# Kernel tuning notes

Hardware: AMD Instinct MI355X
Metric: run time of the kernel (lower is better)

The kernel has to match this reference:

```python
import jax, jax.numpy as jnp
import numpy as np

IN_FEATURES = 256
OUT_FEATURES = 512
NUM_SEGMENTS = 8
GRID_MIN, GRID_MAX = -1.0, 1.0
STEP = (GRID_MAX - GRID_MIN) / NUM_SEGMENTS
LN_EPS = 1e-5


def setup_inputs() -> dict:
    key = jax.random.key(0)
    k1, k2 = jax.random.split(key)
    B = 2048
    x = jax.random.normal(k1, (B, IN_FEATURES), dtype=jnp.float32)
    # Xavier-uniform a_embed, zeros b_embed, as in reset_parameters
    vocab = IN_FEATURES * NUM_SEGMENTS
    limit = float(np.sqrt(6.0 / (vocab + OUT_FEATURES)))
    a_weight = jax.random.uniform(k2, (vocab, OUT_FEATURES), minval=-limit, maxval=limit, dtype=jnp.float32)
    b_weight = jnp.zeros((vocab, OUT_FEATURES), dtype=jnp.float32)
    gamma = jnp.ones((IN_FEATURES,), dtype=jnp.float32)
    beta = jnp.zeros((IN_FEATURES,), dtype=jnp.float32)
    return {"x": x, "a_weight": a_weight, "b_weight": b_weight, "gamma": gamma, "beta": beta}


def reference(x, a_weight, b_weight, gamma, beta):
    # LayerNorm over in_features
    mu = jnp.mean(x, axis=-1, keepdims=True)
    var = jnp.mean(jnp.square(x - mu), axis=-1, keepdims=True)
    xn = (x - mu) * jax.lax.rsqrt(var + LN_EPS) * gamma + beta  # [B, I]

    # data-dependent segment index (torch .long() truncates; clamp makes trunc==floor here)
    float_idx = (xn - GRID_MIN) / STEP
    seg = jnp.clip(float_idx.astype(jnp.int32), 0, NUM_SEGMENTS - 1)  # [B, I]
    global_idx = seg + jnp.arange(IN_FEATURES, dtype=jnp.int32)[None, :] * NUM_SEGMENTS

    a_vals = a_weight[global_idx]  # [B, I, O]
    b_vals = b_weight[global_idx]  # [B, I, O]
    # sum over in_features of a*x + b
    y = jnp.einsum('bi,bio->bo', xn, a_vals) + jnp.sum(b_vals, axis=1)
    return y
```

## Files before the change

### kernel.cpp

```cpp
#include <hip/hip_runtime.h>

#define I_FEAT 256
#define O_FEAT 512
#define NSEG   8
#define KDIM   (I_FEAT * NSEG)
#define KTOT   (2 * KDIM)
#define KC_N   (KTOT / 32)

typedef _Float16 half8   __attribute__((ext_vector_type(8)));
typedef float    floatx4 __attribute__((ext_vector_type(4)));
typedef uint32_t uintx4  __attribute__((ext_vector_type(4)));

__global__ __launch_bounds__(256) void ln_meta(
    const float* __restrict__ x,
    const float* __restrict__ gamma,
    const float* __restrict__ beta,
    uint32_t* __restrict__ meta_g,
    int Bn)
{
    __shared__ float s_psum[4];
    __shared__ float s_psq[4];

    const int tid  = threadIdx.x;
    const int row0 = blockIdx.x * 2;
    const int wave = tid >> 6;
    const int lr   = tid >> 7;
    const int lt   = tid & 127;
    const int row  = row0 + lr;

    float v0 = 0.f, v1 = 0.f;
    if (row < Bn) {
        const float* xr = x + (size_t)row * I_FEAT;
        v0 = xr[lt];
        v1 = xr[lt + 128];
    }
    float sum = v0 + v1;
    float sq  = v0 * v0 + v1 * v1;
    #pragma unroll
    for (int d = 32; d > 0; d >>= 1) {
        sum += __shfl_down(sum, d);
        sq  += __shfl_down(sq, d);
    }
    if ((tid & 63) == 0) { s_psum[wave] = sum; s_psq[wave] = sq; }
    __syncthreads();
    if (row >= Bn) return;

    const float fsum = s_psum[2 * lr] + s_psum[2 * lr + 1];
    const float fsq  = s_psq[2 * lr]  + s_psq[2 * lr + 1];
    const float mu   = fsum * (1.0f / I_FEAT);
    const float var  = fsq * (1.0f / I_FEAT) - mu * mu;
    const float rs   = rsqrtf(var + 1e-5f);

    uint32_t* mr = meta_g + (size_t)row * I_FEAT;
    #pragma unroll
    for (int h = 0; h < 2; ++h) {
        const int f = lt + h * 128;
        const float v = h ? v1 : v0;
        float xn = (v - mu) * rs * gamma[f] + beta[f];
        float fi = (xn + 1.0f) * 4.0f;
        int seg = (int)fi;
        seg = seg < 0 ? 0 : (seg > NSEG - 1 ? NSEG - 1 : seg);
        _Float16 hx = (_Float16)xn;
        uint32_t hb = (uint32_t)__builtin_bit_cast(unsigned short, hx);
        mr[f] = ((uint32_t)seg << 16) | hb;
    }
}

__global__ __launch_bounds__(256) void pack_bfrag(
    const float* __restrict__ Aw,
    const float* __restrict__ Bw,
    uint4* __restrict__ Bf)
{
    __shared__ unsigned short T[64][72];
    const int t  = threadIdx.x;
    const int n0 = blockIdx.x * 64;
    const int k0 = blockIdx.y * 64;
    const float* src = (k0 < KDIM) ? (Aw + (size_t)k0 * O_FEAT)
                                   : (Bw + (size_t)(k0 - KDIM) * O_FEAT);

    #pragma unroll
    for (int s = 0; s < 4; ++s) {
        int e  = s * 1024 + t * 4;
        int kl = e >> 6, nl = e & 63;
        const float4 v = *(const float4*)(src + (size_t)kl * O_FEAT + n0 + nl);
        T[nl + 0][kl] = __builtin_bit_cast(unsigned short, (_Float16)v.x);
        T[nl + 1][kl] = __builtin_bit_cast(unsigned short, (_Float16)v.y);
        T[nl + 2][kl] = __builtin_bit_cast(unsigned short, (_Float16)v.z);
        T[nl + 3][kl] = __builtin_bit_cast(unsigned short, (_Float16)v.w);
    }
    __syncthreads();

    const int lane = t & 63, lane16 = lane & 15, quad = lane >> 4;
    const int sub  = t >> 6;
    #pragma unroll
    for (int f = 0; f < 2; ++f) {
        const int combo = sub * 2 + f;
        const int n16g  = combo & 3;
        const int kch   = combo >> 2;
        const int nl = n16g * 16 + lane16;
        const int kl = kch * 32 + quad * 8;
        const uint4 val = *(const uint4*)&T[nl][kl];
        const int n16t = (n0 >> 4) + n16g;
        const int kc   = (k0 >> 5) + kch;
        Bf[((size_t)n16t * KC_N + kc) * 64 + lane] = val;
    }
}

__global__ __launch_bounds__(256) void am_pack(
    const uint32_t* __restrict__ meta_g,
    uint2* __restrict__ Am,
    int Bn, int mt16Tot)
{
    const int gid  = blockIdx.x * 256 + threadIdx.x;
    const int lane = gid & 63;
    const int pc   = gid >> 6;
    const int kcp  = pc & 63;
    const int mt16 = pc >> 6;
    if (mt16 >= mt16Tot) return;
    const int m    = mt16 * 16 + (lane & 15);
    const int quad = lane >> 4;

    uint2 v = make_uint2(0u, 0u);
    if (m < Bn) {
        const uint32_t* mr = meta_g + (size_t)m * I_FEAT;
        #pragma unroll
        for (int h = 0; h < 2; ++h) {
            const int w    = (kcp * 2 + h) * 4 + quad;
            const int part = w >> 8;
            const int i    = w & 255;
            const uint32_t u = mr[i];
            const uint32_t val = part ? ((u & 0xFFFF0000u) | 0x3C00u) : u;
            if (h == 0) v.x = val; else v.y = val;
        }
    }
    Am[gid] = v;
}

static __device__ __forceinline__ half8 build_onehot(uint32_t u) {
    const uint32_t xb  = u & 0xFFFFu;
    const uint32_t seg = u >> 16;
    const uint64_t oh  = (uint64_t)xb << ((seg & 3u) << 4);
    const uint64_t lo  = (seg < 4u) ? oh : 0ull;
    const uint64_t hi  = (seg < 4u) ? 0ull : oh;
    uintx4 w;
    w[0] = (uint32_t)lo; w[1] = (uint32_t)(lo >> 32);
    w[2] = (uint32_t)hi; w[3] = (uint32_t)(hi >> 32);
    return __builtin_bit_cast(half8, w);
}

__global__ __launch_bounds__(256, 4) void kan_gemm(
    const uint2* __restrict__ Am,
    const uint4* __restrict__ Bf,
    float* __restrict__ out,
    int Bn)
{
    __shared__ float s_red[3][16][64];

    const int t      = threadIdx.x;
    const int wave   = t >> 6, lane = t & 63;
    const int lane16 = lane & 15, quad = lane >> 4;
    const int bid    = blockIdx.x;
    const int ot     = bid & 15;
    const int rt     = bid >> 4;

    const uint2* pa0 = Am + ((size_t)(rt * 2 + 0) * 64) * 64 + lane;
    const uint2* pa1 = Am + ((size_t)(rt * 2 + 1) * 64) * 64 + lane;
    const uint4* pb0 = Bf + ((size_t)(ot * 2 + 0) * KC_N) * 64 + lane;
    const uint4* pb1 = Bf + ((size_t)(ot * 2 + 1) * KC_N) * 64 + lane;

    floatx4 acc[2][2] = {};
    const int kcp0 = wave * 16;

    #pragma unroll 4
    for (int p = 0; p < 16; ++p) {
        const int kcp = kcp0 + p;
        const uint2 u0   = pa0[(size_t)kcp * 64];
        const uint2 u1   = pa1[(size_t)kcp * 64];
        const uint4 bv00 = pb0[(size_t)(2 * kcp + 0) * 64];
        const uint4 bv01 = pb0[(size_t)(2 * kcp + 1) * 64];
        const uint4 bv10 = pb1[(size_t)(2 * kcp + 0) * 64];
        const uint4 bv11 = pb1[(size_t)(2 * kcp + 1) * 64];
        {
            const half8 a0 = build_onehot(u0.x);
            const half8 a1 = build_onehot(u1.x);
            const half8 b0 = __builtin_bit_cast(half8, bv00);
            const half8 b1 = __builtin_bit_cast(half8, bv10);
            acc[0][0] = __builtin_amdgcn_mfma_f32_16x16x32_f16(a0, b0, acc[0][0], 0, 0, 0);
            acc[0][1] = __builtin_amdgcn_mfma_f32_16x16x32_f16(a0, b1, acc[0][1], 0, 0, 0);
            acc[1][0] = __builtin_amdgcn_mfma_f32_16x16x32_f16(a1, b0, acc[1][0], 0, 0, 0);
            acc[1][1] = __builtin_amdgcn_mfma_f32_16x16x32_f16(a1, b1, acc[1][1], 0, 0, 0);
        }
        {
            const half8 a0 = build_onehot(u0.y);
            const half8 a1 = build_onehot(u1.y);
            const half8 b0 = __builtin_bit_cast(half8, bv01);
            const half8 b1 = __builtin_bit_cast(half8, bv11);
            acc[0][0] = __builtin_amdgcn_mfma_f32_16x16x32_f16(a0, b0, acc[0][0], 0, 0, 0);
            acc[0][1] = __builtin_amdgcn_mfma_f32_16x16x32_f16(a0, b1, acc[0][1], 0, 0, 0);
            acc[1][0] = __builtin_amdgcn_mfma_f32_16x16x32_f16(a1, b0, acc[1][0], 0, 0, 0);
            acc[1][1] = __builtin_amdgcn_mfma_f32_16x16x32_f16(a1, b1, acc[1][1], 0, 0, 0);
        }
    }

    if (wave != 0) {
        #pragma unroll
        for (int sm = 0; sm < 2; ++sm)
            #pragma unroll
            for (int sn = 0; sn < 2; ++sn)
                #pragma unroll
                for (int r = 0; r < 4; ++r)
                    s_red[wave - 1][(sm * 2 + sn) * 4 + r][lane] = acc[sm][sn][r];
    }
    __syncthreads();
    if (wave == 0) {
        #pragma unroll
        for (int sm = 0; sm < 2; ++sm) {
            #pragma unroll
            for (int sn = 0; sn < 2; ++sn) {
                #pragma unroll
                for (int r = 0; r < 4; ++r) {
                    const int idx = (sm * 2 + sn) * 4 + r;
                    const float v = acc[sm][sn][r]
                                  + s_red[0][idx][lane]
                                  + s_red[1][idx][lane]
                                  + s_red[2][idx][lane];
                    const int grow = rt * 32 + sm * 16 + quad * 4 + r;
                    const int gcol = ot * 32 + sn * 16 + lane16;
                    if (grow < Bn)
                        out[(size_t)grow * O_FEAT + gcol] = v;
                }
            }
        }
    }
}

extern "C" void kernel_launch(void* const* d_in, const int* in_sizes, int n_in,
                              void* d_out, int out_size, void* d_ws, size_t ws_size,
                              hipStream_t stream) {
    const float* x   = (const float*)d_in[0];
    const float* Aw  = (const float*)d_in[1];
    const float* Bw  = (const float*)d_in[2];
    const float* gam = (const float*)d_in[3];
    const float* bet = (const float*)d_in[4];
    float* out       = (float*)d_out;

    const int Bn       = in_sizes[0] / I_FEAT;
    const int rt32Tot  = (Bn + 31) / 32;
    const int mt16Tot  = rt32Tot * 2;

    uint4* Bf        = (uint4*)d_ws;
    uint2* Am        = (uint2*)(Bf + (size_t)(O_FEAT / 16) * KC_N * 64);
    uint32_t* meta_g = (uint32_t*)(Am + (size_t)mt16Tot * 64 * 64);

    hipLaunchKernelGGL(ln_meta, dim3((Bn + 1) / 2), dim3(256), 0, stream,
                       x, gam, bet, meta_g, Bn);
    hipLaunchKernelGGL(pack_bfrag, dim3(O_FEAT / 64, KTOT / 64), dim3(256), 0, stream,
                       Aw, Bw, Bf);
    hipLaunchKernelGGL(am_pack, dim3(mt16Tot * 16), dim3(256), 0, stream,
                       meta_g, Am, Bn, mt16Tot);
    hipLaunchKernelGGL(kan_gemm, dim3(16 * rt32Tot), dim3(256), 0, stream,
                       Am, Bf, out, Bn);
}
```

Baseline: 91.38 us.

## Fuse prep kernels into one launch and enlarge GEMM row tile to 64

Merges the LayerNorm/meta, weight-fragment packing and A-fragment packing kernels into a single launch. Different block ranges do weight packing or row normalisation plus A packing through shared memory, which removes the meta_g round trip and two launches. The GEMM now computes 64 rows per block instead of 32, reusing each B fragment across four A tiles. It also adds a block-index swizzle for L2 locality, a reduction in which all waves share the epilogue, and launch bounds lowered to 2. The larger tile raises register pressure and cuts the number of blocks, which may hurt occupancy.

```diff
diff --git a/kernel.cpp b/kernel.cpp
--- a/kernel.cpp
+++ b/kernel.cpp
@@ -11,129 +11,118 @@
 typedef float    floatx4 __attribute__((ext_vector_type(4)));
 typedef uint32_t uintx4  __attribute__((ext_vector_type(4)));
 
-__global__ __launch_bounds__(256) void ln_meta(
+__global__ __launch_bounds__(256) void prep(
     const float* __restrict__ x,
+    const float* __restrict__ Aw,
+    const float* __restrict__ Bw,
     const float* __restrict__ gamma,
     const float* __restrict__ beta,
-    uint32_t* __restrict__ meta_g,
-    int Bn)
+    uint4* __restrict__ Bf,
+    uint2* __restrict__ Am,
+    int Bn, int pbTot)
 {
-    __shared__ float s_psum[4];
-    __shared__ float s_psq[4];
-
-    const int tid  = threadIdx.x;
-    const int row0 = blockIdx.x * 2;
-    const int wave = tid >> 6;
-    const int lr   = tid >> 7;
-    const int lt   = tid & 127;
-    const int row  = row0 + lr;
-
-    float v0 = 0.f, v1 = 0.f;
-    if (row < Bn) {
-        const float* xr = x + (size_t)row * I_FEAT;
-        v0 = xr[lt];
-        v1 = xr[lt + 128];
-    }
-    float sum = v0 + v1;
-    float sq  = v0 * v0 + v1 * v1;
-    #pragma unroll
-    for (int d = 32; d > 0; d >>= 1) {
-        sum += __shfl_down(sum, d);
-        sq  += __shfl_down(sq, d);
-    }
-    if ((tid & 63) == 0) { s_psum[wave] = sum; s_psq[wave] = sq; }
-    __syncthreads();
-    if (row >= Bn) return;
-
-    const float fsum = s_psum[2 * lr] + s_psum[2 * lr + 1];
-    const float fsq  = s_psq[2 * lr]  + s_psq[2 * lr + 1];
-    const float mu   = fsum * (1.0f / I_FEAT);
-    const float var  = fsq * (1.0f / I_FEAT) - mu * mu;
-    const float rs   = rsqrtf(var + 1e-5f);
-
-    uint32_t* mr = meta_g + (size_t)row * I_FEAT;
-    #pragma unroll
-    for (int h = 0; h < 2; ++h) {
-        const int f = lt + h * 128;
-        const float v = h ? v1 : v0;
-        float xn = (v - mu) * rs * gamma[f] + beta[f];
-        float fi = (xn + 1.0f) * 4.0f;
-        int seg = (int)fi;
-        seg = seg < 0 ? 0 : (seg > NSEG - 1 ? NSEG - 1 : seg);
-        _Float16 hx = (_Float16)xn;
-        uint32_t hb = (uint32_t)__builtin_bit_cast(unsigned short, hx);
-        mr[f] = ((uint32_t)seg << 16) | hb;
-    }
-}
-
-__global__ __launch_bounds__(256) void pack_bfrag(
-    const float* __restrict__ Aw,
-    const float* __restrict__ Bw,
-    uint4* __restrict__ Bf)
-{
-    __shared__ unsigned short T[64][72];
-    const int t  = threadIdx.x;
-    const int n0 = blockIdx.x * 64;
-    const int k0 = blockIdx.y * 64;
-    const float* src = (k0 < KDIM) ? (Aw + (size_t)k0 * O_FEAT)
-                                   : (Bw + (size_t)(k0 - KDIM) * O_FEAT);
-
-    #pragma unroll
-    for (int s = 0; s < 4; ++s) {
-        int e  = s * 1024 + t * 4;
-        int kl = e >> 6, nl = e & 63;
-        const float4 v = *(const float4*)(src + (size_t)kl * O_FEAT + n0 + nl);
-        T[nl + 0][kl] = __builtin_bit_cast(unsigned short, (_Float16)v.x);
-        T[nl + 1][kl] = __builtin_bit_cast(unsigned short, (_Float16)v.y);
-        T[nl + 2][kl] = __builtin_bit_cast(unsigned short, (_Float16)v.z);
-        T[nl + 3][kl] = __builtin_bit_cast(unsigned short, (_Float16)v.w);
-    }
-    __syncthreads();
-
-    const int lane = t & 63, lane16 = lane & 15, quad = lane >> 4;
-    const int sub  = t >> 6;
-    #pragma unroll
-    for (int f = 0; f < 2; ++f) {
-        const int combo = sub * 2 + f;
-        const int n16g  = combo & 3;
-        const int kch   = combo >> 2;
-        const int nl = n16g * 16 + lane16;
-        const int kl = kch * 32 + quad * 8;
-        const uint4 val = *(const uint4*)&T[nl][kl];
-        const int n16t = (n0 >> 4) + n16g;
-        const int kc   = (k0 >> 5) + kch;
-        Bf[((size_t)n16t * KC_N + kc) * 64 + lane] = val;
-    }
-}
-
-__global__ __launch_bounds__(256) void am_pack(
-    const uint32_t* __restrict__ meta_g,
-    uint2* __restrict__ Am,
-    int Bn, int mt16Tot)
-{
-    const int gid  = blockIdx.x * 256 + threadIdx.x;
-    const int lane = gid & 63;
-    const int pc   = gid >> 6;
-    const int kcp  = pc & 63;
-    const int mt16 = pc >> 6;
-    if (mt16 >= mt16Tot) return;
-    const int m    = mt16 * 16 + (lane & 15);
-    const int quad = lane >> 4;
-
-    uint2 v = make_uint2(0u, 0u);
-    if (m < Bn) {
-        const uint32_t* mr = meta_g + (size_t)m * I_FEAT;
-        #pragma unroll
-        for (int h = 0; h < 2; ++h) {
-            const int w    = (kcp * 2 + h) * 4 + quad;
-            const int part = w >> 8;
-            const int i    = w & 255;
-            const uint32_t u = mr[i];
-            const uint32_t val = part ? ((u & 0xFFFF0000u) | 0x3C00u) : u;
-            if (h == 0) v.x = val; else v.y = val;
-        }
-    }
-    Am[gid] = v;
+    __shared__ char smem[16 * 260 * 4];
+    const int t   = threadIdx.x;
+    const int bid = blockIdx.x;
+
+    if (bid < pbTot) {
+        unsigned short (*T)[72] = (unsigned short(*)[72])smem;
+        const int n0 = (bid & 7) * 64;
+        const int k0 = (bid >> 3) * 64;
+        const float* src = (k0 < KDIM) ? (Aw + (size_t)k0 * O_FEAT)
+                                       : (Bw + (size_t)(k0 - KDIM) * O_FEAT);
+        #pragma unroll
+        for (int s = 0; s < 4; ++s) {
+            int e  = s * 1024 + t * 4;
+            int kl = e >> 6, nl = e & 63;
+            const float4 v = *(const float4*)(src + (size_t)kl * O_FEAT + n0 + nl);
+            T[nl + 0][kl] = __builtin_bit_cast(unsigned short, (_Float16)v.x);
+            T[nl + 1][kl] = __builtin_bit_cast(unsigned short, (_Float16)v.y);
+            T[nl + 2][kl] = __builtin_bit_cast(unsigned short, (_Float16)v.z);
+            T[nl + 3][kl] = __builtin_bit_cast(unsigned short, (_Float16)v.w);
+        }
+        __syncthreads();
+
+        const int lane = t & 63, lane16 = lane & 15, quad = lane >> 4;
+        const int sub  = t >> 6;
+        #pragma unroll
+        for (int f = 0; f < 2; ++f) {
+            const int combo = sub * 2 + f;
+            const int n16g  = combo & 3;
+            const int kch   = combo >> 2;
+            const int nl = n16g * 16 + lane16;
+            const int kl = kch * 32 + quad * 8;
+            const uint4 val = *(const uint4*)&T[nl][kl];
+            const int n16t = (n0 >> 4) + n16g;
+            const int kc   = (k0 >> 5) + kch;
+            Bf[((size_t)n16t * KC_N + kc) * 64 + lane] = val;
+        }
+    } else {
+        uint32_t (*M)[260] = (uint32_t(*)[260])smem;
+        const int mt16 = bid - pbTot;
+        const int rr   = t >> 4;
+        const int c16  = t & 15;
+        const int row  = mt16 * 16 + rr;
+        const bool ok  = (row < Bn);
+
+        float4 v[4];
+        const float* xr = x + (size_t)row * I_FEAT + c16 * 16;
+        #pragma unroll
+        for (int j = 0; j < 4; ++j)
+            v[j] = ok ? *(const float4*)(xr + j * 4) : make_float4(0.f, 0.f, 0.f, 0.f);
+
+        float sum = 0.f, sq = 0.f;
+        #pragma unroll
+        for (int j = 0; j < 4; ++j) {
+            sum += v[j].x + v[j].y + v[j].z + v[j].w;
+            sq  += v[j].x * v[j].x + v[j].y * v[j].y
+                 + v[j].z * v[j].z + v[j].w * v[j].w;
+        }
+        #pragma unroll
+        for (int mask = 1; mask < 16; mask <<= 1) {
+            sum += __shfl_xor(sum, mask);
+            sq  += __shfl_xor(sq,  mask);
+        }
+        const float mu  = sum * (1.0f / I_FEAT);
+        const float var = sq * (1.0f / I_FEAT) - mu * mu;
+        const float rs  = rsqrtf(var + 1e-5f);
+
+        #pragma unroll
+        for (int j = 0; j < 4; ++j) {
+            const float4 g4 = *(const float4*)(gamma + c16 * 16 + j * 4);
+            const float4 b4 = *(const float4*)(beta  + c16 * 16 + j * 4);
+            const float vv[4] = { v[j].x, v[j].y, v[j].z, v[j].w };
+            const float gg[4] = { g4.x, g4.y, g4.z, g4.w };
+            const float bb[4] = { b4.x, b4.y, b4.z, b4.w };
+            #pragma unroll
+            for (int e = 0; e < 4; ++e) {
+                const int c = c16 * 16 + j * 4 + e;
+                float xn = (vv[e] - mu) * rs * gg[e] + bb[e];
+                float fi = (xn + 1.0f) * 4.0f;
+                int seg = (int)fi;
+                seg = seg < 0 ? 0 : (seg > NSEG - 1 ? NSEG - 1 : seg);
+                _Float16 hx = (_Float16)xn;
+                M[rr][c] = ((uint32_t)seg << 16)
+                         | (uint32_t)__builtin_bit_cast(unsigned short, hx);
+            }
+        }
+        __syncthreads();
+
+        const int lane = t & 63, g = t >> 6;
+        const int m_local = lane & 15, quad = lane >> 4;
+        uint2* dst = Am + (size_t)mt16 * 64 * 64 + lane;
+        #pragma unroll
+        for (int kk = 0; kk < 16; ++kk) {
+            const int kcp = g * 16 + kk;
+            const int w0  = kcp * 8 + quad;
+            const int w1  = w0 + 4;
+            const uint32_t u0 = M[m_local][w0 & 255];
+            const uint32_t u1 = M[m_local][w1 & 255];
+            const uint32_t a  = (w0 >> 8) ? ((u0 & 0xFFFF0000u) | 0x3C00u) : u0;
+            const uint32_t b  = (w1 >> 8) ? ((u1 & 0xFFFF0000u) | 0x3C00u) : u1;
+            dst[(size_t)kcp * 64] = make_uint2(a, b);
+        }
+    }
 }
 
 static __device__ __forceinline__ half8 build_onehot(uint32_t u) {
@@ -148,88 +137,104 @@
     return __builtin_bit_cast(half8, w);
 }
 
-__global__ __launch_bounds__(256, 4) void kan_gemm(
+__global__ __launch_bounds__(256, 2) void kan_gemm(
     const uint2* __restrict__ Am,
     const uint4* __restrict__ Bf,
     float* __restrict__ out,
-    int Bn)
+    int Bn, int rt64Tot)
 {
-    __shared__ float s_red[3][16][64];
+    __shared__ floatx4 s_red[4][8][64];
 
     const int t      = threadIdx.x;
     const int wave   = t >> 6, lane = t & 63;
     const int lane16 = lane & 15, quad = lane >> 4;
     const int bid    = blockIdx.x;
-    const int ot     = bid & 15;
-    const int rt     = bid >> 4;
-
-    const uint2* pa0 = Am + ((size_t)(rt * 2 + 0) * 64) * 64 + lane;
-    const uint2* pa1 = Am + ((size_t)(rt * 2 + 1) * 64) * 64 + lane;
-    const uint4* pb0 = Bf + ((size_t)(ot * 2 + 0) * KC_N) * 64 + lane;
-    const uint4* pb1 = Bf + ((size_t)(ot * 2 + 1) * KC_N) * 64 + lane;
-
-    floatx4 acc[2][2] = {};
+
+    int ot, rt;
+    if (rt64Tot == 32) {
+        const int xc = bid & 7, j = bid >> 3;
+        ot = ((j >> 4) << 2) | (xc & 3);
+        rt = (j & 15) | ((xc >> 2) << 4);
+    } else {
+        ot = bid & 15;
+        rt = bid >> 4;
+    }
+
+    const uint2* pa = Am + (size_t)(rt * 4) * 64 * 64 + lane;
+    const uint4* pb = Bf + (size_t)(ot * 2) * KC_N * 64 + lane;
+
+    floatx4 acc[4][2] = {};
     const int kcp0 = wave * 16;
 
     #pragma unroll 4
     for (int p = 0; p < 16; ++p) {
         const int kcp = kcp0 + p;
-        const uint2 u0   = pa0[(size_t)kcp * 64];
-        const uint2 u1   = pa1[(size_t)kcp * 64];
-        const uint4 bv00 = pb0[(size_t)(2 * kcp + 0) * 64];
-        const uint4 bv01 = pb0[(size_t)(2 * kcp + 1) * 64];
-        const uint4 bv10 = pb1[(size_t)(2 * kcp + 0) * 64];
-        const uint4 bv11 = pb1[(size_t)(2 * kcp + 1) * 64];
+        const uint2 u0 = pa[(size_t)kcp * 64];
+        const uint2 u1 = pa[(size_t)(4096  + kcp * 64)];
+        const uint2 u2 = pa[(size_t)(8192  + kcp * 64)];
+        const uint2 u3 = pa[(size_t)(12288 + kcp * 64)];
+        const uint4 b00 = pb[(size_t)(2 * kcp + 0) * 64];
+        const uint4 b01 = pb[(size_t)(2 * kcp + 1) * 64];
+        const uint4 b10 = pb[(size_t)(8192 + (2 * kcp + 0) * 64)];
+        const uint4 b11 = pb[(size_t)(8192 + (2 * kcp + 1) * 64)];
         {
-            const half8 a0 = build_onehot(u0.x);
-            const half8 a1 = build_onehot(u1.x);
-            const half8 b0 = __builtin_bit_cast(half8, bv00);
-            const half8 b1 = __builtin_bit_cast(half8, bv10);
-            acc[0][0] = __builtin_amdgcn_mfma_f32_16x16x32_f16(a0, b0, acc[0][0], 0, 0, 0);
-            acc[0][1] = __builtin_amdgcn_mfma_f32_16x16x32_f16(a0, b1, acc[0][1], 0, 0, 0);
-            acc[1][0] = __builtin_amdgcn_mfma_f32_16x16x32_f16(a1, b0, acc[1][0], 0, 0, 0);
-            acc[1][1] = __builtin_amdgcn_mfma_f32_16x16x32_f16(a1, b1, acc[1][1], 0, 0, 0);
+            const half8 n0 = __builtin_bit_cast(half8, b00);
+            const half8 n1 = __builtin_bit_cast(half8, b10);
+            half8 a;
+            a = build_onehot(u0.x);
+            acc[0][0] = __builtin_amdgcn_mfma_f32_16x16x32_f16(a, n0, acc[0][0], 0, 0, 0);
+            acc[0][1] = __builtin_amdgcn_mfma_f32_16x16x32_f16(a, n1, acc[0][1], 0, 0, 0);
+            a = build_onehot(u1.x);
+            acc[1][0] = __builtin_amdgcn_mfma_f32_16x16x32_f16(a, n0, acc[1][0], 0, 0, 0);
+            acc[1][1] = __builtin_amdgcn_mfma_f32_16x16x32_f16(a, n1, acc[1][1], 0, 0, 0);
+            a = build_onehot(u2.x);
+            acc[2][0] = __builtin_amdgcn_mfma_f32_16x16x32_f16(a, n0, acc[2][0], 0, 0, 0);
+            acc[2][1] = __builtin_amdgcn_mfma_f32_16x16x32_f16(a, n1, acc[2][1], 0, 0, 0);
+            a = build_onehot(u3.x);
+            acc[3][0] = __builtin_amdgcn_mfma_f32_16x16x32_f16(a, n0, acc[3][0], 0, 0, 0);
+            acc[3][1] = __builtin_amdgcn_mfma_f32_16x16x32_f16(a, n1, acc[3][1], 0, 0, 0);
         }
         {
-            const half8 a0 = build_onehot(u0.y);
-            const half8 a1 = build_onehot(u1.y);
-            const half8 b0 = __builtin_bit_cast(half8, bv01);
-            const half8 b1 = __builtin_bit_cast(half8, bv11);
-            acc[0][0] = __builtin_amdgcn_mfma_f32_16x16x32_f16(a0, b0, acc[0][0], 0, 0, 0);
-            acc[0][1] = __builtin_amdgcn_mfma_f32_16x16x32_f16(a0, b1, acc[0][1], 0, 0, 0);
-            acc[1][0] = __builtin_amdgcn_mfma_f32_16x16x32_f16(a1, b0, acc[1][0], 0, 0, 0);
-            acc[1][1] = __builtin_amdgcn_mfma_f32_16x16x32_f16(a1, b1, acc[1][1], 0, 0, 0);
-        }
-    }
-
-    if (wave != 0) {
-        #pragma unroll
-        for (int sm = 0; sm < 2; ++sm)
-            #pragma unroll
-            for (int sn = 0; sn < 2; ++sn)
-                #pragma unroll
-                for (int r = 0; r < 4; ++r)
-                    s_red[wave - 1][(sm * 2 + sn) * 4 + r][lane] = acc[sm][sn][r];
-    }
+            const half8 n0 = __builtin_bit_cast(half8, b01);
+            const half8 n1 = __builtin_bit_cast(half8, b11);
+            half8 a;
+            a = build_onehot(u0.y);
+            acc[0][0] = __builtin_amdgcn_mfma_f32_16x16x32_f16(a, n0, acc[0][0], 0, 0, 0);
+            acc[0][1] = __builtin_amdgcn_mfma_f32_16x16x32_f16(a, n1, acc[0][1], 0, 0, 0);
+            a = build_onehot(u1.y);
+            acc[1][0] = __builtin_amdgcn_mfma_f32_16x16x32_f16(a, n0, acc[1][0], 0, 0, 0);
+            acc[1][1] = __builtin_amdgcn_mfma_f32_16x16x32_f16(a, n1, acc[1][1], 0, 0, 0);
+            a = build_onehot(u2.y);
+            acc[2][0] = __builtin_amdgcn_mfma_f32_16x16x32_f16(a, n0, acc[2][0], 0, 0, 0);
+            acc[2][1] = __builtin_amdgcn_mfma_f32_16x16x32_f16(a, n1, acc[2][1], 0, 0, 0);
+            a = build_onehot(u3.y);
+            acc[3][0] = __builtin_amdgcn_mfma_f32_16x16x32_f16(a, n0, acc[3][0], 0, 0, 0);
+            acc[3][1] = __builtin_amdgcn_mfma_f32_16x16x32_f16(a, n1, acc[3][1], 0, 0, 0);
+        }
+    }
+
+    #pragma unroll
+    for (int mi = 0; mi < 4; ++mi)
+        #pragma unroll
+        for (int ni = 0; ni < 2; ++ni)
+            s_red[wave][mi * 2 + ni][lane] = acc[mi][ni];
     __syncthreads();
-    if (wave == 0) {
-        #pragma unroll
-        for (int sm = 0; sm < 2; ++sm) {
-            #pragma unroll
-            for (int sn = 0; sn < 2; ++sn) {
-                #pragma unroll
-                for (int r = 0; r < 4; ++r) {
-                    const int idx = (sm * 2 + sn) * 4 + r;
-                    const float v = acc[sm][sn][r]
-                                  + s_red[0][idx][lane]
-                                  + s_red[1][idx][lane]
-                                  + s_red[2][idx][lane];
-                    const int grow = rt * 32 + sm * 16 + quad * 4 + r;
-                    const int gcol = ot * 32 + sn * 16 + lane16;
-                    if (grow < Bn)
-                        out[(size_t)grow * O_FEAT + gcol] = v;
-                }
-            }
+
+    #pragma unroll
+    for (int q = 0; q < 2; ++q) {
+        const int tt = wave * 2 + q;
+        const int mi = tt >> 1, ni = tt & 1;
+        floatx4 vsum = s_red[0][tt][lane];
+        vsum += s_red[1][tt][lane];
+        vsum += s_red[2][tt][lane];
+        vsum += s_red[3][tt][lane];
+        const int gcol = ot * 32 + ni * 16 + lane16;
+        const int gr0  = rt * 64 + mi * 16 + quad * 4;
+        #pragma unroll
+        for (int r = 0; r < 4; ++r) {
+            const int grow = gr0 + r;
+            if (grow < Bn)
+                out[(size_t)grow * O_FEAT + gcol] = vsum[r];
         }
     }
 }
@@ -244,20 +249,16 @@
     const float* bet = (const float*)d_in[4];
     float* out       = (float*)d_out;
 
-    const int Bn       = in_sizes[0] / I_FEAT;
-    const int rt32Tot  = (Bn + 31) / 32;
-    const int mt16Tot  = rt32Tot * 2;
-
-    uint4* Bf        = (uint4*)d_ws;
-    uint2* Am        = (uint2*)(Bf + (size_t)(O_FEAT / 16) * KC_N * 64);
-    uint32_t* meta_g = (uint32_t*)(Am + (size_t)mt16Tot * 64 * 64);
-
-    hipLaunchKernelGGL(ln_meta, dim3((Bn + 1) / 2), dim3(256), 0, stream,
-                       x, gam, bet, meta_g, Bn);
-    hipLaunchKernelGGL(pack_bfrag, dim3(O_FEAT / 64, KTOT / 64), dim3(256), 0, stream,
-                       Aw, Bw, Bf);
-    hipLaunchKernelGGL(am_pack, dim3(mt16Tot * 16), dim3(256), 0, stream,
-                       meta_g, Am, Bn, mt16Tot);
-    hipLaunchKernelGGL(kan_gemm, dim3(16 * rt32Tot), dim3(256), 0, stream,
-                       Am, Bf, out, Bn);
-}
+    const int Bn      = in_sizes[0] / I_FEAT;
+    const int mt16Tot = (Bn + 15) / 16;
+    const int rt64Tot = (Bn + 63) / 64;
+    const int pbTot   = (O_FEAT / 64) * (KTOT / 64);
+
+    uint4* Bf = (uint4*)d_ws;
+    uint2* Am = (uint2*)(Bf + (size_t)(O_FEAT / 16) * KC_N * 64);
+
+    hipLaunchKernelGGL(prep, dim3(pbTot + mt16Tot), dim3(256), 0, stream,
+                       x, Aw, Bw, gam, bet, Bf, Am, Bn, pbTot);
+    hipLaunchKernelGGL(kan_gemm, dim3(16 * rt64Tot), dim3(256), 0, stream,
+                       Am, Bf, out, Bn, rt64Tot);
+}
```

Result: faster. 87.82 us (-3.9%).
